# Kernel tuning notes

Measured on AMD Instinct MI355X. Metric: run time of the kernel, lower is better.

## Reference

```python
import jax, jax.numpy as jnp
import numpy as np

NUM = 512
SIGMA = 0.2

def approx_heaviside(x):
    # ApproxHeaviside forward: hard step (0/1); sigma only affects the surrogate gradient.
    return (x > 0).astype(x.dtype)

def setup_inputs() -> dict:
    key = jax.random.key(0)
    k1, k2 = jax.random.split(key)
    inputs = jax.random.normal(k1, (8, 4096, NUM), dtype=jnp.float32)
    w = jax.random.normal(k2, (NUM, NUM), dtype=jnp.float32) * 0.02
    b = jnp.zeros((NUM,), dtype=jnp.float32)
    return {"inputs": inputs, "w": w, "b": b}

def reference(inputs, w, b):
    # zero the diagonal of w (fill_diagonal_(0))
    w1 = w * (1.0 - jnp.eye(NUM, dtype=w.dtype))
    # inhib = rinputs @ w1 + b over all tokens, vectorized
    inhib = jnp.einsum('bsn,nm->bsm', inputs, w1) + b
    gate = approx_heaviside(inhib)
    # diag_embed(inhib) then matmul == elementwise multiply by the gate
    return inputs * gate
```

## Files before the change

### kernel.cpp

```cpp
#include <hip/hip_runtime.h>
#include <stdint.h>


#define NUMD 512
#define EPS 1e-3f
#define FIXCAP (1u << 20)
#define LCAP 2048u
#define SA 4096.0f
#define SW 8192.0f
#define INV_S (1.0f / 33554432.0f)
#define TILE_F16 4096
#define SLAB_F16 (16 * TILE_F16)

typedef _Float16 f16;
typedef _Float16 f16x8 __attribute__((ext_vector_type(8)));
typedef float    f32x4 __attribute__((ext_vector_type(4)));

#define GLOAD_LDS16(g, l)                                                      \
  __builtin_amdgcn_global_load_lds(                                            \
      (const __attribute__((address_space(1))) void*)(g),                      \
      (__attribute__((address_space(3))) void*)(l), 16, 0, 0)

__global__ __launch_bounds__(256) void prep(
    const float* __restrict__ W, float* __restrict__ Wt,
    f16* __restrict__ WtH, f16* __restrict__ WtL, unsigned* __restrict__ cnt)
{
    const int n = blockIdx.x;
    if (n == 0 && threadIdx.x == 0) *cnt = 0;
    const int slab = n >> 7, rn = n & 127;
    const int srow = (rn >> 1) & 3;
    for (int k = threadIdx.x; k < NUMD; k += 256) {
        float v = W[(size_t)k * NUMD + n];
        if (k == n) v = 0.0f;
        Wt[(size_t)n * NUMD + k] = v;
        const float vs = v * SW;
        f16 h  = (f16)vs;
        f16 lo = (f16)(vs - (float)h);
        const int kt = k >> 5, kk = k & 31, c = kk >> 3, e = kk & 7;
        const int p = c ^ srow;
        const size_t off = (size_t)slab * SLAB_F16 + (size_t)kt * TILE_F16
                         + rn * 32 + p * 8 + e;
        WtH[off] = h; WtL[off] = lo;
    }
}

__global__ __launch_bounds__(256, 2) void li_mfma(
    const float* __restrict__ A,
    const f16* __restrict__ WtH, const f16* __restrict__ WtL,
    const float* __restrict__ bias,
    float* __restrict__ out,
    unsigned* __restrict__ cnt, unsigned* __restrict__ list,
    int M, int cpx)
{
    __shared__ __align__(16) f16 lds[2][4][128][32];
    __shared__ unsigned lcnt, lbase;

    const int tid = threadIdx.x;
    const int l   = tid & 63;
    const int wv  = tid >> 6;
    const int wr  = wv >> 1;
    const int wc  = wv & 1;
    const int lG  = l >> 4;
    const int lM  = l & 15;

    int w = blockIdx.x;
    if (cpx) { const int xcd = w & 7, c = w >> 3; w = xcd * cpx + c; }
    const int m0  = (w >> 2) * 128;
    const int n0b = (w & 3) * 128;

    const size_t bOff = ((size_t)(n0b >> 7) * SLAB_F16) * 2 + wv * 2048 + l * 16;
    const char* pBH = (const char*)WtH;
    const char* pBL = (const char*)WtL;

#define STAGE_B(nb, ktb) do {                                                  \
    GLOAD_LDS16(pBH + bOff + (ktb),        &lds[nb][2][wv * 32][0]);           \
    GLOAD_LDS16(pBH + bOff + (ktb) + 1024, &lds[nb][2][wv * 32 + 16][0]);      \
    GLOAD_LDS16(pBL + bOff + (ktb),        &lds[nb][3][wv * 32][0]);           \
    GLOAD_LDS16(pBL + bOff + (ktb) + 1024, &lds[nb][3][wv * 32 + 16][0]);      \
  } while (0)

    const int r0 = tid >> 2, ca = tid & 3;
    const int r1 = r0 + 64;
    const float* aBase0 = A + (size_t)(m0 + r0) * NUMD + ca * 8;
    const float* aBase1 = A + (size_t)(m0 + r1) * NUMD + ca * 8;
    const int wo0 = r0 * 64 + ((ca ^ ((r0 >> 1) & 3)) << 4);
    const int wo1 = r1 * 64 + ((ca ^ ((r1 >> 1) & 3)) << 4);

    float4 av00, av01, av10, av11;

#define ALOAD(kt) do {                                                         \
    const float* s0 = aBase0 + (size_t)(kt) * 32;                              \
    const float* s1 = aBase1 + (size_t)(kt) * 32;                              \
    av00 = *(const float4*)s0; av01 = *(const float4*)(s0 + 4);                \
    av10 = *(const float4*)s1; av11 = *(const float4*)(s1 + 4);                \
  } while (0)

#define ACONV(nb) do {                                                         \
    const float a0[8] = {av00.x, av00.y, av00.z, av00.w,                       \
                         av01.x, av01.y, av01.z, av01.w};                      \
    const float a1[8] = {av10.x, av10.y, av10.z, av10.w,                       \
                         av11.x, av11.y, av11.z, av11.w};                      \
    f16x8 h0, lo0, h1, lo1;                                                    \
    _Pragma("unroll")                                                          \
    for (int e = 0; e < 8; ++e) {                                              \
        float as0 = a0[e] * SA; f16 hv0 = (f16)as0;                            \
        h0[e] = hv0; lo0[e] = (f16)(as0 - (float)hv0);                         \
        float as1 = a1[e] * SA; f16 hv1 = (f16)as1;                            \
        h1[e] = hv1; lo1[e] = (f16)(as1 - (float)hv1);                         \
    }                                                                          \
    *(f16x8*)((char*)&lds[nb][0][0][0] + wo0) = h0;                            \
    *(f16x8*)((char*)&lds[nb][1][0][0] + wo0) = lo0;                           \
    *(f16x8*)((char*)&lds[nb][0][0][0] + wo1) = h1;                            \
    *(f16x8*)((char*)&lds[nb][1][0][0] + wo1) = lo1;                           \
  } while (0)

    int aRd[4], bRd[4];
#pragma unroll
    for (int f = 0; f < 4; ++f) {
        const int mr = wr * 64 + f * 16 + lM;
        aRd[f] = mr * 64 + ((lG ^ ((mr >> 1) & 3)) << 4);
        const int nr = wc * 64 + f * 16 + lM;
        bRd[f] = nr * 64 + ((lG ^ ((nr >> 1) & 3)) << 4);
    }

    f32x4 acc[4][4];
#pragma unroll
    for (int i = 0; i < 4; ++i)
#pragma unroll
        for (int j = 0; j < 4; ++j) acc[i][j] = f32x4{0.f, 0.f, 0.f, 0.f};

    ALOAD(0);
    STAGE_B(0, 0);
    ACONV(0);

    const int NT = NUMD / 32;
    for (int kt = 0; kt < NT; ++kt) {
        const int cur = kt & 1;
        __syncthreads();

        if (kt + 1 < NT) {
            STAGE_B(cur ^ 1, (size_t)(kt + 1) * 8192);
            ALOAD(kt + 1);
        }

        const char* PAH = (const char*)&lds[cur][0][0][0];
        const char* PAL = (const char*)&lds[cur][1][0][0];
        const char* PBH = (const char*)&lds[cur][2][0][0];
        const char* PBL = (const char*)&lds[cur][3][0][0];

        f16x8 bh[4], bl[4];
#pragma unroll
        for (int fj = 0; fj < 4; ++fj) {
            bh[fj] = *(const f16x8*)(PBH + bRd[fj]);
            bl[fj] = *(const f16x8*)(PBL + bRd[fj]);
        }
        __builtin_amdgcn_s_setprio(1);
#pragma unroll
        for (int fi = 0; fi < 4; ++fi) {
            const f16x8 ah = *(const f16x8*)(PAH + aRd[fi]);
            const f16x8 al = *(const f16x8*)(PAL + aRd[fi]);
#pragma unroll
            for (int fj = 0; fj < 4; ++fj) {
                acc[fi][fj] = __builtin_amdgcn_mfma_f32_16x16x32_f16(ah, bh[fj], acc[fi][fj], 0, 0, 0);
                acc[fi][fj] = __builtin_amdgcn_mfma_f32_16x16x32_f16(ah, bl[fj], acc[fi][fj], 0, 0, 0);
                acc[fi][fj] = __builtin_amdgcn_mfma_f32_16x16x32_f16(al, bh[fj], acc[fi][fj], 0, 0, 0);
            }
        }
        __builtin_amdgcn_s_setprio(0);

        if (kt + 1 < NT) ACONV(cur ^ 1);
    }

    __syncthreads();
    unsigned* lbuf = (unsigned*)&lds[0][0][0][0];
    if (tid == 0) lcnt = 0;
    __syncthreads();

#pragma unroll
    for (int fj = 0; fj < 4; ++fj) {
        const int n = n0b + wc * 64 + fj * 16 + lM;
        const float bvj = bias[n];
#pragma unroll
        for (int fi = 0; fi < 4; ++fi) {
            const int mb = m0 + wr * 64 + fi * 16 + lG * 4;
#pragma unroll
            for (int r = 0; r < 4; ++r) {
                const size_t idx = (size_t)(mb + r) * NUMD + n;
                const float inh = acc[fi][fj][r] * INV_S + bvj;
                const float x = A[idx];
                out[idx] = (inh > 0.0f) ? x : 0.0f;
                if (__builtin_fabsf(inh) <= EPS) {
                    unsigned p = atomicAdd(&lcnt, 1u);
                    if (p < LCAP) lbuf[p] = (unsigned)idx;
                }
            }
        }
    }

    __syncthreads();
    if (tid == 0) {
        unsigned nf = lcnt; if (nf > LCAP) nf = LCAP;
        lbase = atomicAdd(cnt, nf);
    }
    __syncthreads();
    {
        unsigned nf = lcnt; if (nf > LCAP) nf = LCAP;
        for (unsigned i = tid; i < nf; i += 256) {
            const unsigned p = lbase + i;
            if (p < FIXCAP) list[p] = lbuf[i];
        }
    }
#undef STAGE_B
#undef ALOAD
#undef ACONV
}

__global__ __launch_bounds__(256) void fixup(
    const float* __restrict__ A, const float* __restrict__ Wt,
    const float* __restrict__ bias, float* __restrict__ out,
    const unsigned* __restrict__ cnt, const unsigned* __restrict__ list,
    unsigned total)
{
    unsigned nfix = *cnt;
    if (nfix > FIXCAP) nfix = FIXCAP;
    for (unsigned e = blockIdx.x * blockDim.x + threadIdx.x; e < nfix;
         e += gridDim.x * blockDim.x) {
        const unsigned code = list[e];
        if (code >= total) continue;
        const int n = (int)(code & 511);
        const float* ar = A  + (size_t)(code >> 9) * NUMD;
        const float* wr = Wt + (size_t)n * NUMD;
        float s = 0.0f;
#pragma unroll 8
        for (int k = 0; k < NUMD; ++k)
            s = fmaf(ar[k], wr[k], s);
        const float inh = s + bias[n];
        out[code] = (inh > 0.0f) ? A[code] : 0.0f;
    }
}

#define BM 128
#define BN 256
#define BK 16
#define TM 8
#define TN 16
#define NTF (NUMD / BK)

__global__ __launch_bounds__(256) void zero_diag_kernel(
    const float* __restrict__ W, float* __restrict__ Wz)
{
    const int f = (int)(blockIdx.x * blockDim.x + threadIdx.x) * 4;
    const int row = f >> 9, col0 = f & 511;
    float4 v = *(const float4*)(W + f);
    if (row == col0 + 0) v.x = 0.0f;
    if (row == col0 + 1) v.y = 0.0f;
    if (row == col0 + 2) v.z = 0.0f;
    if (row == col0 + 3) v.w = 0.0f;
    *(float4*)(Wz + f) = v;
}

template<bool ZDIAG>
__global__ __launch_bounds__(256, 1) void li_gemm_fp32(
    const float* __restrict__ A, const float* __restrict__ Wm,
    const float* __restrict__ bias, float* __restrict__ out, int M)
{
    __shared__ __align__(16) float As[2][BM][BK];
    __shared__ __align__(16) float Bs[2][BK][BN];
    const int tid = threadIdx.x, lane = tid & 63, wv = tid >> 6;
    const int tc = tid & 15, tr = tid >> 4;
    const int m0 = blockIdx.x * BM, n0 = blockIdx.y * BN;
    const int am0 = wv * 32 + (lane >> 2), am1 = am0 + 16;
    const int q0 = ((lane & 3) ^ ((am0 >> 3) & 3)) << 2;
    const int q1 = ((lane & 3) ^ ((am1 >> 3) & 3)) << 2;
    const float* aSrc0 = A + (size_t)(m0 + am0) * NUMD + q0;
    const float* aSrc1 = A + (size_t)(m0 + am1) * NUMD + q1;
    const float* wSrc = Wm + (size_t)(wv * 4) * NUMD + n0 + lane * 4;
    float acc[TM][TN];
#pragma unroll
    for (int i = 0; i < TM; ++i)
#pragma unroll
        for (int j = 0; j < TN; ++j) acc[i][j] = 0.0f;
    GLOAD_LDS16(aSrc0, &As[0][wv * 32][0]);
    GLOAD_LDS16(aSrc1, &As[0][wv * 32 + 16][0]);
#pragma unroll
    for (int r = 0; r < 4; ++r)
        GLOAD_LDS16(wSrc + (size_t)r * NUMD, &Bs[0][wv * 4 + r][0]);
    aSrc0 += BK; aSrc1 += BK; wSrc += (size_t)BK * NUMD;
    for (int kt = 0; kt < NTF; ++kt) {
        const int cur = kt & 1;
        __syncthreads();
        if (kt + 1 < NTF) {
            const int nb = cur ^ 1;
            GLOAD_LDS16(aSrc0, &As[nb][wv * 32][0]);
            GLOAD_LDS16(aSrc1, &As[nb][wv * 32 + 16][0]);
#pragma unroll
            for (int r = 0; r < 4; ++r)
                GLOAD_LDS16(wSrc + (size_t)r * NUMD, &Bs[nb][wv * 4 + r][0]);
            aSrc0 += BK; aSrc1 += BK; wSrc += (size_t)BK * NUMD;
        }
        if (ZDIAG) {
            const int kk = kt * BK;
            if (tid < BK) {
                const int col = kk + tid - n0;
                if (col >= 0 && col < BN) Bs[cur][tid][col] = 0.0f;
            }
            __syncthreads();
        }
#pragma unroll
        for (int g = 0; g < 4; ++g) {
            float4 af[TM];
#pragma unroll
            for (int i = 0; i < TM; ++i) {
                const int m = tr * TM + i;
                af[i] = *(const float4*)&As[cur][m][(g ^ ((m >> 3) & 3)) << 2];
            }
#pragma unroll
            for (int dk = 0; dk < 4; ++dk) {
                float b[TN];
#pragma unroll
                for (int c = 0; c < 4; ++c) {
                    float4 b4 = *(const float4*)&Bs[cur][g * 4 + dk][tc * 4 + 64 * c];
                    b[4*c+0] = b4.x; b[4*c+1] = b4.y; b[4*c+2] = b4.z; b[4*c+3] = b4.w;
                }
#pragma unroll
                for (int i = 0; i < TM; ++i) {
                    const float a = ((const float*)&af[i])[dk];
#pragma unroll
                    for (int j = 0; j < TN; ++j) acc[i][j] = fmaf(a, b[j], acc[i][j]);
                }
            }
        }
    }
    float bv[TN];
#pragma unroll
    for (int c = 0; c < 4; ++c) {
        float4 b4 = *(const float4*)(bias + n0 + tc * 4 + 64 * c);
        bv[4*c+0] = b4.x; bv[4*c+1] = b4.y; bv[4*c+2] = b4.z; bv[4*c+3] = b4.w;
    }
#pragma unroll
    for (int i = 0; i < TM; ++i) {
        const int gm = m0 + tr * TM + i;
        const float* inrow = A + (size_t)gm * NUMD + n0 + tc * 4;
        float* orow = out + (size_t)gm * NUMD + n0 + tc * 4;
#pragma unroll
        for (int c = 0; c < 4; ++c) {
            float4 x = *(const float4*)(inrow + 64 * c);
            float4 o;
            o.x = (acc[i][4*c+0] + bv[4*c+0] > 0.0f) ? x.x : 0.0f;
            o.y = (acc[i][4*c+1] + bv[4*c+1] > 0.0f) ? x.y : 0.0f;
            o.z = (acc[i][4*c+2] + bv[4*c+2] > 0.0f) ? x.z : 0.0f;
            o.w = (acc[i][4*c+3] + bv[4*c+3] > 0.0f) ? x.w : 0.0f;
            *(float4*)(orow + 64 * c) = o;
        }
    }
}

extern "C" void kernel_launch(void* const* d_in, const int* in_sizes, int n_in,
                              void* d_out, int out_size, void* d_ws, size_t ws_size,
                              hipStream_t stream) {
    const float* A    = (const float*)d_in[0];
    const float* W    = (const float*)d_in[1];
    const float* bias = (const float*)d_in[2];
    float* out        = (float*)d_out;
    const int M = in_sizes[0] / NUMD;

    const size_t need = (2u << 20) + 1024 + 4 * (size_t)FIXCAP + 4096;

    if (ws_size >= need) {
        char* wsb = (char*)d_ws;
        float*    Wt   = (float*)wsb;
        f16*      WtH  = (f16*)(wsb + (1u << 20));
        f16*      WtL  = (f16*)(wsb + (1u << 20) + (512u << 10));
        unsigned* cnt  = (unsigned*)(wsb + (2u << 20));
        unsigned* list = cnt + 256;

        prep<<<dim3(NUMD), 256, 0, stream>>>(W, Wt, WtH, WtL, cnt);
        const int nwg = (M / 128) * (NUMD / 128);
        const int cpx = (nwg % 8 == 0) ? (nwg / 8) : 0;
        li_mfma<<<dim3(nwg), 256, 0, stream>>>(A, WtH, WtL, bias, out,
                                               cnt, list, M, cpx);
        fixup<<<dim3(256), 256, 0, stream>>>(A, Wt, bias, out, cnt, list,
                                             (unsigned)((size_t)M * NUMD));
    } else {
        dim3 grid(M / BM, NUMD / BN);
        const size_t wbytes = (size_t)NUMD * NUMD * sizeof(float);
        if (ws_size >= wbytes) {
            float* Wz = (float*)d_ws;
            zero_diag_kernel<<<dim3(NUMD * NUMD / (4 * 256)), 256, 0, stream>>>(W, Wz);
            li_gemm_fp32<false><<<grid, 256, 0, stream>>>(A, Wz, bias, out, M);
        } else {
            li_gemm_fp32<true><<<grid, 256, 0, stream>>>(A, W, bias, out, M);
        }
    }
}
```

Baseline: 230.8 us.

## Fuse near-threshold fp32 fixup into GEMM epilogue via LDS-staged coalesced stores

Removes the separate fixup kernel and global list/counter. Near-zero gate candidates are recomputed in exact fp32 inside each GEMM workgroup after its tile is written. The epilogue now stages accumulators through LDS so the A reads and output writes are coalesced float4 accesses instead of strided scalar ones. This saves a kernel launch and the global atomics, at the cost of tail imbalance in workgroups with many candidates and a per-block cap of 512 fixups. Entries past the cap are silently dropped.

```diff
diff --git a/kernel.cpp b/kernel.cpp
--- a/kernel.cpp
+++ b/kernel.cpp
@@ -4,8 +4,7 @@
 
 #define NUMD 512
 #define EPS 1e-3f
-#define FIXCAP (1u << 20)
-#define LCAP 2048u
+#define FLCAP 512u
 #define SA 4096.0f
 #define SW 8192.0f
 #define INV_S (1.0f / 33554432.0f)
@@ -23,10 +22,9 @@
 
 __global__ __launch_bounds__(256) void prep(
     const float* __restrict__ W, float* __restrict__ Wt,
-    f16* __restrict__ WtH, f16* __restrict__ WtL, unsigned* __restrict__ cnt)
+    f16* __restrict__ WtH, f16* __restrict__ WtL)
 {
     const int n = blockIdx.x;
-    if (n == 0 && threadIdx.x == 0) *cnt = 0;
     const int slab = n >> 7, rn = n & 127;
     const int srow = (rn >> 1) & 3;
     for (int k = threadIdx.x; k < NUMD; k += 256) {
@@ -47,13 +45,14 @@
 __global__ __launch_bounds__(256, 2) void li_mfma(
     const float* __restrict__ A,
     const f16* __restrict__ WtH, const f16* __restrict__ WtL,
+    const float* __restrict__ Wt,
     const float* __restrict__ bias,
     float* __restrict__ out,
-    unsigned* __restrict__ cnt, unsigned* __restrict__ list,
     int M, int cpx)
 {
     __shared__ __align__(16) f16 lds[2][4][128][32];
-    __shared__ unsigned lcnt, lbase;
+    __shared__ unsigned flist[FLCAP];
+    __shared__ unsigned lcnt;
 
     const int tid = threadIdx.x;
     const int l   = tid & 63;
@@ -172,71 +171,61 @@
     }
 
     __syncthreads();
-    unsigned* lbuf = (unsigned*)&lds[0][0][0][0];
+    float* cbuf = (float*)&lds[0][0][0][0];
     if (tid == 0) lcnt = 0;
+
+#pragma unroll
+    for (int fj = 0; fj < 4; ++fj) {
+        const int cl = wc * 64 + fj * 16 + lM;
+#pragma unroll
+        for (int fi = 0; fi < 4; ++fi) {
+            const int rl = wr * 64 + fi * 16 + lG * 4;
+#pragma unroll
+            for (int r = 0; r < 4; ++r)
+                cbuf[(rl + r) * 128 + cl] = acc[fi][fj][r] * INV_S;
+        }
+    }
     __syncthreads();
 
-#pragma unroll
-    for (int fj = 0; fj < 4; ++fj) {
-        const int n = n0b + wc * 64 + fj * 16 + lM;
-        const float bvj = bias[n];
-#pragma unroll
-        for (int fi = 0; fi < 4; ++fi) {
-            const int mb = m0 + wr * 64 + fi * 16 + lG * 4;
-#pragma unroll
-            for (int r = 0; r < 4; ++r) {
-                const size_t idx = (size_t)(mb + r) * NUMD + n;
-                const float inh = acc[fi][fj][r] * INV_S + bvj;
-                const float x = A[idx];
-                out[idx] = (inh > 0.0f) ? x : 0.0f;
-                if (__builtin_fabsf(inh) <= EPS) {
-                    unsigned p = atomicAdd(&lcnt, 1u);
-                    if (p < LCAP) lbuf[p] = (unsigned)idx;
-                }
-            }
-        }
+    const int rcol = (tid & 31) * 4;
+    const float4 bv4 = *(const float4*)(bias + n0b + rcol);
+#pragma unroll
+    for (int ch = 0; ch < 16; ++ch) {
+        const int rrow = ch * 8 + (tid >> 5);
+        const float4 v = *(const float4*)&cbuf[rrow * 128 + rcol];
+        const size_t gi = (size_t)(m0 + rrow) * NUMD + n0b + rcol;
+        const float4 x = *(const float4*)(A + gi);
+        const float inh0 = v.x + bv4.x, inh1 = v.y + bv4.y;
+        const float inh2 = v.z + bv4.z, inh3 = v.w + bv4.w;
+        float4 o;
+        o.x = (inh0 > 0.0f) ? x.x : 0.0f;
+        o.y = (inh1 > 0.0f) ? x.y : 0.0f;
+        o.z = (inh2 > 0.0f) ? x.z : 0.0f;
+        o.w = (inh3 > 0.0f) ? x.w : 0.0f;
+        *(float4*)(out + gi) = o;
+        if (__builtin_fabsf(inh0) <= EPS) { unsigned p = atomicAdd(&lcnt, 1u); if (p < FLCAP) flist[p] = (unsigned)(gi + 0); }
+        if (__builtin_fabsf(inh1) <= EPS) { unsigned p = atomicAdd(&lcnt, 1u); if (p < FLCAP) flist[p] = (unsigned)(gi + 1); }
+        if (__builtin_fabsf(inh2) <= EPS) { unsigned p = atomicAdd(&lcnt, 1u); if (p < FLCAP) flist[p] = (unsigned)(gi + 2); }
+        if (__builtin_fabsf(inh3) <= EPS) { unsigned p = atomicAdd(&lcnt, 1u); if (p < FLCAP) flist[p] = (unsigned)(gi + 3); }
     }
 
     __syncthreads();
-    if (tid == 0) {
-        unsigned nf = lcnt; if (nf > LCAP) nf = LCAP;
-        lbase = atomicAdd(cnt, nf);
-    }
-    __syncthreads();
-    {
-        unsigned nf = lcnt; if (nf > LCAP) nf = LCAP;
-        for (unsigned i = tid; i < nf; i += 256) {
-            const unsigned p = lbase + i;
-            if (p < FIXCAP) list[p] = lbuf[i];
-        }
+    unsigned nf = lcnt; if (nf > FLCAP) nf = FLCAP;
+    for (unsigned e = tid; e < nf; e += 256) {
+        const unsigned code = flist[e];
+        const int n = (int)(code & 511);
+        const float* ar  = A  + (size_t)(code >> 9) * NUMD;
+        const float* wr_ = Wt + (size_t)n * NUMD;
+        float s = 0.0f;
+#pragma unroll 8
+        for (int k = 0; k < NUMD; ++k)
+            s = fmaf(ar[k], wr_[k], s);
+        const float inh = s + bias[n];
+        out[code] = (inh > 0.0f) ? A[code] : 0.0f;
     }
 #undef STAGE_B
 #undef ALOAD
 #undef ACONV
-}
-
-__global__ __launch_bounds__(256) void fixup(
-    const float* __restrict__ A, const float* __restrict__ Wt,
-    const float* __restrict__ bias, float* __restrict__ out,
-    const unsigned* __restrict__ cnt, const unsigned* __restrict__ list,
-    unsigned total)
-{
-    unsigned nfix = *cnt;
-    if (nfix > FIXCAP) nfix = FIXCAP;
-    for (unsigned e = blockIdx.x * blockDim.x + threadIdx.x; e < nfix;
-         e += gridDim.x * blockDim.x) {
-        const unsigned code = list[e];
-        if (code >= total) continue;
-        const int n = (int)(code & 511);
-        const float* ar = A  + (size_t)(code >> 9) * NUMD;
-        const float* wr = Wt + (size_t)n * NUMD;
-        float s = 0.0f;
-#pragma unroll 8
-        for (int k = 0; k < NUMD; ++k)
-            s = fmaf(ar[k], wr[k], s);
-        const float inh = s + bias[n];
-        out[code] = (inh > 0.0f) ? A[code] : 0.0f;
-    }
 }
 
 #define BM 128
@@ -364,23 +353,19 @@
     float* out        = (float*)d_out;
     const int M = in_sizes[0] / NUMD;
 
-    const size_t need = (2u << 20) + 1024 + 4 * (size_t)FIXCAP + 4096;
+    const size_t need = (2u << 20) + 4096;
 
     if (ws_size >= need) {
         char* wsb = (char*)d_ws;
-        float*    Wt   = (float*)wsb;
-        f16*      WtH  = (f16*)(wsb + (1u << 20));
-        f16*      WtL  = (f16*)(wsb + (1u << 20) + (512u << 10));
-        unsigned* cnt  = (unsigned*)(wsb + (2u << 20));
-        unsigned* list = cnt + 256;
-
-        prep<<<dim3(NUMD), 256, 0, stream>>>(W, Wt, WtH, WtL, cnt);
+        float* Wt  = (float*)wsb;
+        f16*   WtH = (f16*)(wsb + (1u << 20));
+        f16*   WtL = (f16*)(wsb + (1u << 20) + (512u << 10));
+
+        prep<<<dim3(NUMD), 256, 0, stream>>>(W, Wt, WtH, WtL);
         const int nwg = (M / 128) * (NUMD / 128);
         const int cpx = (nwg % 8 == 0) ? (nwg / 8) : 0;
-        li_mfma<<<dim3(nwg), 256, 0, stream>>>(A, WtH, WtL, bias, out,
-                                               cnt, list, M, cpx);
-        fixup<<<dim3(256), 256, 0, stream>>>(A, Wt, bias, out, cnt, list,
-                                             (unsigned)((size_t)M * NUMD));
+        li_mfma<<<dim3(nwg), 256, 0, stream>>>(A, WtH, WtL, Wt, bias, out,
+                                               M, cpx);
     } else {
         dim3 grid(M / BM, NUMD / BN);
         const size_t wbytes = (size_t)NUMD * NUMD * sizeof(float);
```

Measured after the change: 203.6 us. -11.8%, faster.
